# Optimization experiments

Measured on AMD Instinct MI355X. Metric: run time of the kernel, lower is better.

Reference implementation:

```python
import jax, jax.numpy as jnp
import numpy as np

B, T, D, H = 4, 2048, 1024, 16
DK = D // H

def setup_inputs() -> dict:
    key = jax.random.key(0)
    ks = jax.random.split(key, 9)
    s = 0.02
    return {
        "x": jax.random.normal(ks[0], (B, T, D), dtype=jnp.float32),
        "Wq": jax.random.normal(ks[1], (D, D), dtype=jnp.float32) * s,
        "bq": jnp.zeros((D,), dtype=jnp.float32),
        "Wk": jax.random.normal(ks[2], (D, D), dtype=jnp.float32) * s,
        "bk": jnp.zeros((D,), dtype=jnp.float32),
        "Wv": jax.random.normal(ks[3], (D, D), dtype=jnp.float32) * s,
        "bv": jnp.zeros((D,), dtype=jnp.float32),
        "Wo": jax.random.normal(ks[4], (D, D), dtype=jnp.float32) * s,
        "bo": jnp.zeros((D,), dtype=jnp.float32),
    }

def reference(x, Wq, bq, Wk, bk, Wv, bv, Wo, bo):
    b, t, c = x.shape
    # projections -> [B, H, T, DK]
    def split_heads(y):
        return y.reshape(b, t, H, DK).transpose(0, 2, 1, 3)
    q = split_heads(x @ Wq.T + bq)
    k = split_heads(x @ Wk.T + bk)
    v = split_heads(x @ Wv.T + bv)
    scale = 1.0 / jnp.sqrt(jnp.asarray(DK, dtype=x.dtype))
    scores = jnp.einsum("bhqd,bhkd->bhqk", q, k) * scale  # [B,H,T,T]
    causal = jnp.tril(jnp.ones((t, t), dtype=bool))
    scores = jnp.where(causal, scores, jnp.asarray(-jnp.inf, dtype=scores.dtype))
    attn = jax.nn.softmax(scores, axis=-1)
    out = jnp.einsum("bhqk,bhkd->bhqd", attn, v)  # [B,H,T,DK]
    out = out.transpose(0, 2, 1, 3).reshape(b, t, c)
    return out @ Wo.T + bo
```

## Files before the change

### kernel.cpp

```cpp
#include <hip/hip_runtime.h>
#include <hip/hip_bf16.h>

#define DEV __device__ __forceinline__

typedef unsigned short u16;
typedef unsigned int u32;
typedef __attribute__((ext_vector_type(4))) float f32x4;
typedef __attribute__((ext_vector_type(16))) float f32x16;
typedef __attribute__((ext_vector_type(8))) __bf16 bf16x8;
typedef __attribute__((ext_vector_type(8))) u16 u16x8;
typedef __attribute__((ext_vector_type(4))) u16 u16x4;
typedef __attribute__((ext_vector_type(4))) u32 u32x4;

#define CSCALE 0.18033688011112042f

DEV u16 f2bf(float f) {
    u32 u = __builtin_bit_cast(u32, f);
    u32 r = (u + 0x7fffu + ((u >> 16) & 1u)) >> 16;
    return (u16)r;
}

DEV u16 f2bf_fast(float f) {
    u32 u = __builtin_bit_cast(u32, f);
    return (u16)((u + 0x8000u) >> 16);
}

DEV float fastrcp(float x) {
#if __has_builtin(__builtin_amdgcn_rcpf)
    return __builtin_amdgcn_rcpf(x);
#else
    return 1.0f / x;
#endif
}

DEV u32 cvtpk_bf16(float lo, float hi) {
    u32 r;
    asm("v_cvt_pk_bf16_f32 %0, %1, %2" : "=v"(r) : "v"(lo), "v"(hi));
    return r;
}

DEV void plswap(u32& a, u32& b) {
    asm volatile("v_permlane32_swap_b32 %0, %1" : "+v"(a), "+v"(b));
}

DEV void gload_lds16(const void* g, void* l) {
    void* gg = const_cast<void*>(g);
    __builtin_amdgcn_global_load_lds(
        (const __attribute__((address_space(1))) void*)gg,
        (__attribute__((address_space(3))) void*)l,
        16, 0, 0);
}

DEV f32x16 mfma32(bf16x8 a, bf16x8 b, f32x16 c) {
    return __builtin_amdgcn_mfma_f32_32x32x16_bf16(a, b, c, 0, 0, 0);
}

__global__ void cvt_f32_bf16(const float* __restrict__ in, u16* __restrict__ out,
                             int n4, float scale) {
    int i = blockIdx.x * blockDim.x + threadIdx.x;
    if (i < n4) {
        float4 v = ((const float4*)in)[i];
        u16x4 o;
        o[0] = f2bf(v.x * scale); o[1] = f2bf(v.y * scale);
        o[2] = f2bf(v.z * scale); o[3] = f2bf(v.w * scale);
        ((u16x4*)out)[i] = o;
    }
}

__global__ void build_bias(const float* __restrict__ bq, const float* __restrict__ bk,
                           const float* __restrict__ bv, float* __restrict__ o) {
    int i = blockIdx.x * blockDim.x + threadIdx.x;
    if (i < 3072) {
        float v;
        if (i < 1024) v = bq[i] * CSCALE;
        else if (i < 2048) v = bk[i - 1024];
        else v = bv[i - 2048];
        o[i] = v;
    }
}

template<int F32OUT>
__global__ __launch_bounds__(256) void gemm_bt(
    const u16* __restrict__ A, const u16* __restrict__ B,
    const float* __restrict__ bias, void* __restrict__ Cv,
    int K, int ldc, int bnPerXcd)
{
    __shared__ u16 As[128 * 64];
    __shared__ u16 Bs[128 * 64];
    const int t = threadIdx.x;
    const int lane = t & 63;
    const int w = t >> 6;
    const int wm = w >> 1, wn = w & 1;
    const int id = (int)blockIdx.x;
    const int xcd = id & 7, r = id >> 3;
    const int bm = (r / bnPerXcd) * 128;
    const int bn = (xcd * bnPerXcd + r % bnPerXcd) * 128;
    const int lr = lane & 15;
    const int lg = lane >> 4;
    const int swz = (lr & 7) << 4;

    f32x4 acc[4][4] = {};

    for (int k0 = 0; k0 < K; k0 += 64) {
        #pragma unroll
        for (int i = 0; i < 4; ++i) {
            int idx = t + i * 256;
            int row = idx >> 3;
            int gsrc = (idx & 7) ^ (row & 7);
            gload_lds16((const char*)A + ((size_t)(bm + row) * K + k0 + gsrc * 8) * 2,
                        (char*)As + idx * 16);
            gload_lds16((const char*)B + ((size_t)(bn + row) * K + k0 + gsrc * 8) * 2,
                        (char*)Bs + idx * 16);
        }
        __syncthreads();
        #pragma unroll
        for (int kk = 0; kk < 2; ++kk) {
            bf16x8 af[4], bfr[4];
            #pragma unroll
            for (int m = 0; m < 4; ++m)
                af[m] = *(const bf16x8*)((const char*)As + (wm * 64 + m * 16 + lr) * 128 +
                                         ((kk * 64 + lg * 16) ^ swz));
            #pragma unroll
            for (int n = 0; n < 4; ++n)
                bfr[n] = *(const bf16x8*)((const char*)Bs + (wn * 64 + n * 16 + lr) * 128 +
                                          ((kk * 64 + lg * 16) ^ swz));
            #pragma unroll
            for (int m = 0; m < 4; ++m)
                #pragma unroll
                for (int n = 0; n < 4; ++n)
                    acc[m][n] = __builtin_amdgcn_mfma_f32_16x16x32_bf16(af[m], bfr[n], acc[m][n], 0, 0, 0);
        }
        __syncthreads();
    }

    #pragma unroll
    for (int n = 0; n < 4; ++n) {
        int col = bn + wn * 64 + n * 16 + lr;
        float bv = bias[col];
        #pragma unroll
        for (int m = 0; m < 4; ++m) {
            int row0 = bm + wm * 64 + m * 16 + lg * 4;
            #pragma unroll
            for (int r2 = 0; r2 < 4; ++r2) {
                float v = acc[m][n][r2] + bv;
                size_t idx = (size_t)(row0 + r2) * ldc + col;
                if (F32OUT) ((float*)Cv)[idx] = v;
                else        ((u16*)Cv)[idx] = f2bf(v);
            }
        }
    }
}

__global__ __launch_bounds__(512, 2) void gemm_qkv8(
    const u16* __restrict__ A, const u16* __restrict__ B,
    const float* __restrict__ bias, u16* __restrict__ C,
    int K, int ldc, int ncols)
{
    constexpr int TBUF = 256 * 64;
    __shared__ __align__(16) u16 lds[4 * TBUF >> 1 << 1];
    u16* As = lds;
    u16* Bs = lds + 2 * TBUF;

    const int t = threadIdx.x;
    const int lane = t & 63, w = t >> 6;
    const int wm = w >> 2, wn = w & 3;
    const int lr = lane & 15, lg = lane >> 4;
    const int swz = (lr & 7) << 4;

    const int id = (int)blockIdx.x;
    const int bm = (id / ncols) * 256;
    const int bn = (id % ncols) * 256;
    const int NT = K >> 6;

    const u16* aSrc[4];
    const u16* bSrc[4];
    #pragma unroll
    for (int i = 0; i < 4; ++i) {
        int idx = t + i * 512, row = idx >> 3, g = idx & 7;
        aSrc[i] = A + (size_t)(bm + row) * K + ((g ^ (row & 7)) * 8);
        bSrc[i] = B + (size_t)(bn + row) * K + ((g ^ (row & 7)) * 8);
    }

    f32x4 acc[8][4] = {};

    #pragma unroll
    for (int i = 0; i < 4; ++i) {
        gload_lds16(aSrc[i], As + (t + i * 512) * 8);
        gload_lds16(bSrc[i], Bs + (t + i * 512) * 8);
        aSrc[i] += 64; bSrc[i] += 64;
    }
    asm volatile("s_waitcnt vmcnt(0)" ::: "memory");
    __builtin_amdgcn_s_barrier();

    for (int kt0 = 0; kt0 < NT; kt0 += 2) {
        #pragma unroll
        for (int hh = 0; hh < 2; ++hh) {
            const int BUF = hh;
            const int kt = kt0 + hh;
            const bool more = (kt + 1 < NT);
            const char* Ab = (const char*)(As + BUF * TBUF);
            const char* Bb = (const char*)(Bs + BUF * TBUF);
            u16* An = As + (BUF ^ 1) * TBUF;
            u16* Bn = Bs + (BUF ^ 1) * TBUF;

            bf16x8 bfr[2][4];
            #pragma unroll
            for (int p = 0; p < 4; ++p) {
                if (p == 0) {
                    #pragma unroll
                    for (int kk = 0; kk < 2; ++kk)
                        #pragma unroll
                        for (int n = 0; n < 4; ++n)
                            bfr[kk][n] = *(const bf16x8*)(Bb +
                                (wn * 64 + n * 16 + lr) * 128 + ((kk * 64 + lg * 16) ^ swz));
                }
                bf16x8 af[2][2];
                #pragma unroll
                for (int kk = 0; kk < 2; ++kk)
                    #pragma unroll
                    for (int m2 = 0; m2 < 2; ++m2)
                        af[kk][m2] = *(const bf16x8*)(Ab +
                            (wm * 128 + (p * 2 + m2) * 16 + lr) * 128 + ((kk * 64 + lg * 16) ^ swz));
                if (more && p < 2) {
                    #pragma unroll
                    for (int i = p * 2; i < p * 2 + 2; ++i) {
                        gload_lds16(aSrc[i], An + (t + i * 512) * 8);
                        gload_lds16(bSrc[i], Bn + (t + i * 512) * 8);
                        aSrc[i] += 64; bSrc[i] += 64;
                    }
                }
                __builtin_amdgcn_s_barrier();
                asm volatile("s_waitcnt lgkmcnt(0)" ::: "memory");
                __builtin_amdgcn_s_setprio(1);
                #pragma unroll
                for (int kk = 0; kk < 2; ++kk)
                    #pragma unroll
                    for (int m2 = 0; m2 < 2; ++m2)
                        #pragma unroll
                        for (int n = 0; n < 4; ++n)
                            acc[p * 2 + m2][n] = __builtin_amdgcn_mfma_f32_16x16x32_bf16(
                                af[kk][m2], bfr[kk][n], acc[p * 2 + m2][n], 0, 0, 0);
                __builtin_amdgcn_s_setprio(0);
                if (p == 3 && more)
                    asm volatile("s_waitcnt vmcnt(0)" ::: "memory");
                __builtin_amdgcn_s_barrier();
            }
        }
    }

    const int wcol = bn + wn * 64;
    float bv[4];
    #pragma unroll
    for (int n = 0; n < 4; ++n) bv[n] = bias[wcol + n * 16 + lr];
    u16* ot = lds + w * (64 * 72);
    const int rowR = lane >> 1, segC = (lane & 1) * 32;
    #pragma unroll
    for (int pass = 0; pass < 2; ++pass) {
        if (pass) { asm volatile("s_waitcnt lgkmcnt(0)" ::: "memory"); __builtin_amdgcn_s_barrier(); }
        #pragma unroll
        for (int mm = 0; mm < 4; ++mm)
            #pragma unroll
            for (int n = 0; n < 4; ++n)
                #pragma unroll
                for (int r = 0; r < 4; ++r)
                    ot[(mm * 16 + lg * 4 + r) * 72 + n * 16 + lr] =
                        f2bf(acc[pass * 4 + mm][n][r] + bv[n]);
        asm volatile("s_waitcnt lgkmcnt(0)" ::: "memory");
        #pragma unroll
        for (int half = 0; half < 2; ++half) {
            int row_l = rowR + half * 32;
            int grow = bm + wm * 128 + pass * 64 + row_l;
            const u16* src = ot + row_l * 72 + segC;
            u16* dst = C + (size_t)grow * ldc + wcol + segC;
            #pragma unroll
            for (int s2 = 0; s2 < 4; ++s2)
                *(u16x8*)(dst + s2 * 8) = *(const u16x8*)(src + s2 * 8);
        }
    }
}

__global__ __launch_bounds__(256, 2) void attn_fwd(
    const u16* __restrict__ QKV, u16* __restrict__ Om)
{
    constexpr int T = 2048, LD = 3072, DO = 1024;
    constexpr int PSTR = 72;
    constexpr float NEG = -3.0e38f;

    __shared__ __align__(16) u16 Ks[2][64 * 64];
    __shared__ __align__(16) u16 Vt[2][64 * PSTR];

    const int t = threadIdx.x, lane = t & 63, w = t >> 6;
    const int ql = lane & 31, hi = lane >> 5;

    const int id = (int)blockIdx.x;
    const int slot = id >> 6;
    const int bh = (id & 7) * 8 + ((id >> 3) & 7);
    const int q0 = (15 - slot) * 128;
    const int b = bh >> 4, h = bh & 15;
    const size_t rowbase = (size_t)b * T * LD + h * 64;
    const u16* Qm = QKV + rowbase;
    const u16* Km = QKV + rowbase + 1024;
    const u16* Vm = QKV + rowbase + 2048;
    const int nt = q0 / 64 + 2;

    const int qg = q0 + w * 32 + ql;
    const int qmax = q0 + w * 32 + 31;

    bf16x8 qf[4];
    {
        const u16* qp = Qm + (size_t)qg * LD + hi * 8;
        #pragma unroll
        for (int s = 0; s < 4; ++s) qf[s] = *(const bf16x8*)(qp + s * 16);
    }

    f32x16 oa[2] = {};
    float lsum = 0.f;

    const int krow = t >> 3, kslot = t & 7;
    const u16* kCur = Km + (size_t)krow * LD + 8 * (kslot ^ (krow & 7));
    const int kv2 = (t & 31) * 2, dd = (t >> 5) * 8;
    const u16* vCur = Vm + (size_t)kv2 * LD + dd;
    u16x8 vva, vvb;

    auto stageK = [&](int buf) {
        u16* dst = (u16*)Ks + buf * 4096 + t * 8;
        gload_lds16(kCur, dst);
        gload_lds16(kCur + 32 * LD, dst + 2048);
        kCur += 64 * LD;
    };
    auto loadV = [&]() {
        vva = *(const u16x8*)vCur;
        vvb = *(const u16x8*)(vCur + LD);
        vCur += 64 * LD;
    };
    auto writeVt = [&](int buf) {
        u32* vd = (u32*)((u16*)Vt + buf * (64 * PSTR) + dd * PSTR + kv2);
        #pragma unroll
        for (int j = 0; j < 8; ++j)
            vd[j * (PSTR / 2)] = (u32)vva[j] | ((u32)vvb[j] << 16);
    };

    stageK(0);
    loadV();
    writeVt(0);

    for (int it0 = 0; it0 < nt; it0 += 2) {
        #pragma unroll
        for (int half = 0; half < 2; ++half) {
            const int BUF = half;
            const int it = it0 + half;
            const int kv0 = it * 64;
            __syncthreads();

            const bool more = (it + 1 < nt);
            if (more) { stageK(BUF ^ 1); loadV(); }

            const bool a0  = kv0 <= qmax;
            const bool a0h = kv0 + 32 <= qmax;

            f32x16 sa[2] = {};
            __builtin_amdgcn_s_setprio(1);
            #pragma unroll
            for (int n = 0; n < 2; ++n) {
                if (!(n ? a0h : a0)) continue;
                const int row = n * 32 + ql;
                const int swz = (row & 7) << 4;
                #pragma unroll
                for (int s = 0; s < 4; ++s) {
                    bf16x8 kf = *(const bf16x8*)((const char*)Ks + BUF * 8192 + row * 128 +
                                                 ((((s << 1) | hi) << 4) ^ swz));
                    sa[n] = mfma32(kf, qf[s], sa[n]);
                }
            }
            __builtin_amdgcn_s_setprio(0);

            u32x4 pw[2][2];
            if (a0) {
                float rs = 0.f;
                #pragma unroll
                for (int n = 0; n < 2; ++n) {
                    if (n == 1 && !a0h) continue;
                    if (kv0 + n * 32 + 31 > q0 + w * 32) {
                        #pragma unroll
                        for (int r = 0; r < 16; ++r) {
                            int kvg = kv0 + n * 32 + (r & 3) + 8 * (r >> 2) + 4 * hi;
                            if (kvg > qg) sa[n][r] = NEG;
                        }
                    }
                    float pv[16];
                    #pragma unroll
                    for (int r = 0; r < 16; ++r)
                        pv[r] = __builtin_exp2f(sa[n][r]);
                    float s8[8];
                    #pragma unroll
                    for (int r = 0; r < 8; ++r) s8[r] = pv[r] + pv[r + 8];
                    rs += ((s8[0] + s8[4]) + (s8[1] + s8[5])) + ((s8[2] + s8[6]) + (s8[3] + s8[7]));
                    #pragma unroll
                    for (int s = 0; s < 2; ++s) {
                        u32 u0 = cvtpk_bf16(pv[8 * s + 0], pv[8 * s + 1]);
                        u32 u1 = cvtpk_bf16(pv[8 * s + 2], pv[8 * s + 3]);
                        u32 u2 = cvtpk_bf16(pv[8 * s + 4], pv[8 * s + 5]);
                        u32 u3 = cvtpk_bf16(pv[8 * s + 6], pv[8 * s + 7]);
                        plswap(u0, u2);
                        plswap(u1, u3);
                        pw[n][s] = u32x4{u0, u1, u2, u3};
                    }
                }
                rs += __shfl_xor(rs, 32);
                lsum += rs;
            }

            __builtin_amdgcn_s_setprio(1);
            #pragma unroll
            for (int dt = 0; dt < 2; ++dt) {
                const int vrow = dt * 32 + ql;
                #pragma unroll
                for (int n = 0; n < 2; ++n) {
                    if (!(n ? a0h : a0)) continue;
                    #pragma unroll
                    for (int s = 0; s < 2; ++s) {
                        bf16x8 vf = *(const bf16x8*)((const u16*)Vt + BUF * (64 * PSTR) +
                                                     vrow * PSTR + n * 32 + s * 16 + hi * 8);
                        oa[dt] = mfma32(vf, __builtin_bit_cast(bf16x8, pw[n][s]), oa[dt]);
                    }
                }
            }
            __builtin_amdgcn_s_setprio(0);

            if (more) writeVt(BUF ^ 1);
        }
    }

    __syncthreads();
    u16* ot = ((u16*)Vt) + w * (32 * PSTR);
    const float inv = fastrcp(lsum);
    #pragma unroll
    for (int dt = 0; dt < 2; ++dt)
        #pragma unroll
        for (int r = 0; r < 16; ++r) {
            int d = dt * 32 + (r & 3) + 8 * (r >> 2) + 4 * hi;
            ot[ql * PSTR + d] = f2bf_fast(oa[dt][r] * inv);
        }
    const int lq = lane >> 1, hv = lane & 1;
    const size_t obase = (size_t)b * T * DO + h * 64;
    const u16* src = ot + lq * PSTR + hv * 32;
    u16* dst = Om + obase + (size_t)(q0 + w * 32 + lq) * DO + hv * 32;
    #pragma unroll
    for (int seg = 0; seg < 4; ++seg)
        *(u16x8*)(dst + seg * 8) = *(const u16x8*)(src + seg * 8);
}

extern "C" void kernel_launch(void* const* d_in, const int* in_sizes, int n_in,
                              void* d_out, int out_size, void* d_ws, size_t ws_size,
                              hipStream_t stream)
{
    const float* x  = (const float*)d_in[0];
    const float* Wq = (const float*)d_in[1];
    const float* bq = (const float*)d_in[2];
    const float* Wk = (const float*)d_in[3];
    const float* bk = (const float*)d_in[4];
    const float* Wv = (const float*)d_in[5];
    const float* bv = (const float*)d_in[6];
    const float* Wo = (const float*)d_in[7];
    const float* bo = (const float*)d_in[8];

    constexpr int T = 2048, D = 1024;
    constexpr size_t MT = (size_t)4 * T;

    const size_t NEED = (size_t)74 << 20;
    if (ws_size < NEED) return;

    char* ws = (char*)d_ws;
    u16* xb    = (u16*)(ws);
    u16* Ob    = (u16*)(ws);
    u16* Wqkvb = (u16*)(ws + ((size_t)16 << 20));
    u16* Wob   = (u16*)(ws + ((size_t)22 << 20));
    u16* QKVb  = (u16*)(ws + ((size_t)24 << 20));
    float* bqkv = (float*)(ws + ((size_t)72 << 20));

    int nx4 = (int)(MT * D / 4);
    cvt_f32_bf16<<<(nx4 + 255) / 256, 256, 0, stream>>>(x, xb, nx4, 1.0f);
    int nw4 = D * D / 4;
    cvt_f32_bf16<<<(nw4 + 255) / 256, 256, 0, stream>>>(Wq, Wqkvb, nw4, CSCALE);
    cvt_f32_bf16<<<(nw4 + 255) / 256, 256, 0, stream>>>(Wk, Wqkvb + (size_t)D * D, nw4, 1.0f);
    cvt_f32_bf16<<<(nw4 + 255) / 256, 256, 0, stream>>>(Wv, Wqkvb + (size_t)2 * D * D, nw4, 1.0f);
    cvt_f32_bf16<<<(nw4 + 255) / 256, 256, 0, stream>>>(Wo, Wob, nw4, 1.0f);
    build_bias<<<12, 256, 0, stream>>>(bq, bk, bv, bqkv);

    gemm_qkv8<<<dim3(384), 512, 0, stream>>>(xb, Wqkvb, bqkv, QKVb, D, 3072, 12);

    attn_fwd<<<dim3(1024), 256, 0, stream>>>(QKVb, Ob);

    gemm_bt<1><<<dim3(512), 256, 0, stream>>>(Ob, Wob, bo, d_out, D, 1024, 1);
}
```

Before: 180.9 us.

## Split QKV GEMM tiles into half-buffers with deeper async prefetch

Restructures the QKV projection GEMM's shared-memory tiles into 128-row halves and issues global-to-LDS loads for A and B halves of future k-tiles up to two steps ahead, using partial vmcnt waits instead of full drains. The per-phase fragment schedule changes so that each wave loads its four A fragments once per half and reuses them across two B sub-tiles. The aim is to hide global load latency better and cut LDS fragment reads per MFMA. The trade-off is more complex buffer-reuse ordering, where a wrong waitcnt count or a buffer overwritten too early could cause races. The lgkmcnt wait before the MFMAs was also removed, which relies on the compiler inserting it.

```diff
diff --git a/kernel.cpp b/kernel.cpp
--- a/kernel.cpp
+++ b/kernel.cpp
@@ -156,40 +156,51 @@
     const float* __restrict__ bias, u16* __restrict__ C,
     int K, int ldc, int ncols)
 {
-    constexpr int TBUF = 256 * 64;
-    __shared__ __align__(16) u16 lds[4 * TBUF >> 1 << 1];
-    u16* As = lds;
-    u16* Bs = lds + 2 * TBUF;
+    constexpr int HS = 128 * 64;
+    __shared__ __align__(16) u16 lds[8 * HS];
+    u16* Asl = lds;
+    u16* Bsl = lds + 4 * HS;
 
     const int t = threadIdx.x;
     const int lane = t & 63, w = t >> 6;
     const int wm = w >> 2, wn = w & 3;
     const int lr = lane & 15, lg = lane >> 4;
-    const int swz = (lr & 7) << 4;
+    const int rsw = (lr & 7) << 4;
 
     const int id = (int)blockIdx.x;
     const int bm = (id / ncols) * 256;
     const int bn = (id % ncols) * 256;
     const int NT = K >> 6;
 
-    const u16* aSrc[4];
-    const u16* bSrc[4];
-    #pragma unroll
-    for (int i = 0; i < 4; ++i) {
-        int idx = t + i * 512, row = idx >> 3, g = idx & 7;
-        aSrc[i] = A + (size_t)(bm + row) * K + ((g ^ (row & 7)) * 8);
-        bSrc[i] = B + (size_t)(bn + row) * K + ((g ^ (row & 7)) * 8);
-    }
+    const u16 *aP0, *aP1, *bP0, *bP1;
+    {
+        int row0 = t >> 3, g0 = t & 7;
+        int row1 = (t + 512) >> 3, g1 = t & 7;
+        aP0 = A + (size_t)(bm + row0) * K + (g0 ^ (row0 & 7)) * 8;
+        aP1 = A + (size_t)(bm + row1) * K + (g1 ^ (row1 & 7)) * 8;
+        bP0 = B + (size_t)(bn + row0) * K + (g0 ^ (row0 & 7)) * 8;
+        bP1 = B + (size_t)(bn + row1) * K + (g1 ^ (row1 & 7)) * 8;
+    }
+    const size_t hstep = (size_t)128 * K;
+
+    auto issueA = [&](int kt, int h) {
+        u16* d = Asl + (((kt & 1) << 1) + h) * HS + t * 8;
+        size_t off = (size_t)h * hstep + (size_t)kt * 64;
+        gload_lds16(aP0 + off, d);
+        gload_lds16(aP1 + off, d + 512 * 8);
+    };
+    auto issueB = [&](int kt, int h) {
+        u16* d = Bsl + (((kt & 1) << 1) + h) * HS + t * 8;
+        size_t off = (size_t)h * hstep + (size_t)kt * 64;
+        gload_lds16(bP0 + off, d);
+        gload_lds16(bP1 + off, d + 512 * 8);
+    };
 
     f32x4 acc[8][4] = {};
 
-    #pragma unroll
-    for (int i = 0; i < 4; ++i) {
-        gload_lds16(aSrc[i], As + (t + i * 512) * 8);
-        gload_lds16(bSrc[i], Bs + (t + i * 512) * 8);
-        aSrc[i] += 64; bSrc[i] += 64;
-    }
-    asm volatile("s_waitcnt vmcnt(0)" ::: "memory");
+    issueA(0, 0); issueB(0, 0); issueA(0, 1); issueB(0, 1);
+    issueB(1, 0); issueA(1, 0); issueA(1, 1);
+    asm volatile("s_waitcnt vmcnt(6)" ::: "memory");
     __builtin_amdgcn_s_barrier();
 
     for (int kt0 = 0; kt0 < NT; kt0 += 2) {
@@ -197,52 +208,60 @@
         for (int hh = 0; hh < 2; ++hh) {
             const int BUF = hh;
             const int kt = kt0 + hh;
-            const bool more = (kt + 1 < NT);
-            const char* Ab = (const char*)(As + BUF * TBUF);
-            const char* Bb = (const char*)(Bs + BUF * TBUF);
-            u16* An = As + (BUF ^ 1) * TBUF;
-            u16* Bn = Bs + (BUF ^ 1) * TBUF;
-
-            bf16x8 bfr[2][4];
+            const char* Ab = (const char*)(Asl + ((BUF << 1) + wm) * HS);
+            const char* Bb = (const char*)(Bsl + ((BUF << 1) + (wn >> 1)) * HS);
+            const int rb = (wn & 1) * 64;
+
+            bf16x8 af[2][4], bfr[2][2][2];
             #pragma unroll
             for (int p = 0; p < 4; ++p) {
+                const int mh = p >> 1, nh = p & 1;
                 if (p == 0) {
+                    #pragma unroll
+                    for (int kk = 0; kk < 2; ++kk) {
+                        #pragma unroll
+                        for (int m = 0; m < 4; ++m)
+                            af[kk][m] = *(const bf16x8*)(Ab + (m * 16 + lr) * 128 +
+                                                         ((kk * 64 + lg * 16) ^ rsw));
+                        #pragma unroll
+                        for (int n = 0; n < 2; ++n)
+                            bfr[0][kk][n] = *(const bf16x8*)(Bb + (rb + n * 16 + lr) * 128 +
+                                                             ((kk * 64 + lg * 16) ^ rsw));
+                    }
+                } else if (p == 1) {
                     #pragma unroll
                     for (int kk = 0; kk < 2; ++kk)
                         #pragma unroll
-                        for (int n = 0; n < 4; ++n)
-                            bfr[kk][n] = *(const bf16x8*)(Bb +
-                                (wn * 64 + n * 16 + lr) * 128 + ((kk * 64 + lg * 16) ^ swz));
+                        for (int n = 0; n < 2; ++n)
+                            bfr[1][kk][n] = *(const bf16x8*)(Bb + (rb + 32 + n * 16 + lr) * 128 +
+                                                             ((kk * 64 + lg * 16) ^ rsw));
+                } else if (p == 2) {
+                    #pragma unroll
+                    for (int kk = 0; kk < 2; ++kk)
+                        #pragma unroll
+                        for (int m = 0; m < 4; ++m)
+                            af[kk][m] = *(const bf16x8*)(Ab + (64 + m * 16 + lr) * 128 +
+                                                         ((kk * 64 + lg * 16) ^ rsw));
                 }
-                bf16x8 af[2][2];
-                #pragma unroll
-                for (int kk = 0; kk < 2; ++kk)
-                    #pragma unroll
-                    for (int m2 = 0; m2 < 2; ++m2)
-                        af[kk][m2] = *(const bf16x8*)(Ab +
-                            (wm * 128 + (p * 2 + m2) * 16 + lr) * 128 + ((kk * 64 + lg * 16) ^ swz));
-                if (more && p < 2) {
-                    #pragma unroll
-                    for (int i = p * 2; i < p * 2 + 2; ++i) {
-                        gload_lds16(aSrc[i], An + (t + i * 512) * 8);
-                        gload_lds16(bSrc[i], Bn + (t + i * 512) * 8);
-                        aSrc[i] += 64; bSrc[i] += 64;
-                    }
-                }
+                if (p == 0)      { if (kt + 1 < NT) issueB(kt + 1, 1); }
+                else if (p == 2) { if (kt + 2 < NT) issueB(kt + 2, 0); }
+                else if (p == 3) { if (kt + 2 < NT) { issueA(kt + 2, 0); issueA(kt + 2, 1); } }
+
                 __builtin_amdgcn_s_barrier();
-                asm volatile("s_waitcnt lgkmcnt(0)" ::: "memory");
                 __builtin_amdgcn_s_setprio(1);
                 #pragma unroll
                 for (int kk = 0; kk < 2; ++kk)
                     #pragma unroll
-                    for (int m2 = 0; m2 < 2; ++m2)
+                    for (int m = 0; m < 4; ++m)
                         #pragma unroll
-                        for (int n = 0; n < 4; ++n)
-                            acc[p * 2 + m2][n] = __builtin_amdgcn_mfma_f32_16x16x32_bf16(
-                                af[kk][m2], bfr[kk][n], acc[p * 2 + m2][n], 0, 0, 0);
+                        for (int n = 0; n < 2; ++n)
+                            acc[mh * 4 + m][nh * 2 + n] = __builtin_amdgcn_mfma_f32_16x16x32_bf16(
+                                af[kk][m], bfr[nh][kk][n], acc[mh * 4 + m][nh * 2 + n], 0, 0, 0);
                 __builtin_amdgcn_s_setprio(0);
-                if (p == 3 && more)
-                    asm volatile("s_waitcnt vmcnt(0)" ::: "memory");
+                if (p == 3) {
+                    if (kt + 2 < NT) asm volatile("s_waitcnt vmcnt(6)" ::: "memory");
+                    else             asm volatile("s_waitcnt vmcnt(0)" ::: "memory");
+                }
                 __builtin_amdgcn_s_barrier();
             }
         }
```

Result: slower. 184.8 us, median of 3 (+2.1%).
